# Performance work log

Hardware: AMD Instinct MI355X
Metric: run time of the kernel (lower is better)

The kernel has to match this reference:

```python
import jax, jax.numpy as jnp
import numpy as np

B, S, H, NH, DK, VOCAB, FF, L = 512, 64, 512, 8, 64, 2000, 2048, 6


def _pos_enc():
    pos = jnp.arange(S, dtype=jnp.float32)[:, None]           # [S,1]
    i = jnp.arange(H // 2, dtype=jnp.float32)                  # [H/2]
    ang = pos / (10000.0 ** (2.0 * i / H))                     # [S,H/2]
    pe = jnp.zeros((S, H), jnp.float32)
    pe = pe.at[:, 0::2].set(jnp.sin(ang)).at[:, 1::2].set(jnp.cos(ang))
    return pe


def _ln(x, g, b, eps=1e-5):
    m = x.mean(-1, keepdims=True)
    v = ((x - m) ** 2).mean(-1, keepdims=True)
    return (x - m) / jnp.sqrt(v + eps) * g + b


def _heads(x, w):  # x:[B,S,H] w:[H,H] -> [B,NH,S,DK]
    return (x @ w.T).reshape(B, S, NH, DK).transpose(0, 2, 1, 3)


def _sdpa(Q, K, V, keep):  # keep: bool mask broadcastable to [B,NH,S,S]
    scores = jnp.einsum('bhqd,bhkd->bhqk', Q, K) / np.sqrt(DK).astype(np.float32)
    scores = jnp.where(keep, scores, -1e9)
    return jnp.einsum('bhqk,bhkd->bhqd', jax.nn.softmax(scores, axis=-1), V)


def _merge(z, wo):  # [B,NH,S,DK] -> [B,S,H] -> out proj
    return z.transpose(0, 2, 1, 3).reshape(B, S, H) @ wo.T


def setup_inputs():
    key = jax.random.key(0)
    ks = jax.random.split(key, 30)
    n = lambda k, sh: jax.random.normal(k, sh, jnp.float32) * 0.02
    inp = {
        'source_ids': jax.random.randint(ks[0], (B, S), 0, VOCAB),
        'target_ids': jax.random.randint(ks[1], (B, S), 0, VOCAB),
        'source_mask': jnp.ones((B, S), jnp.int32),
        'target_mask': jnp.ones((B, S), jnp.int32),
        'src_emb': n(ks[2], (VOCAB, H)),
        'tgt_emb': n(ks[3], (VOCAB, H)),
        'enc_wq': n(ks[4], (L, H, H)), 'enc_wk': n(ks[5], (L, H, H)),
        'enc_wv': n(ks[6], (L, H, H)), 'enc_wo': n(ks[7], (L, H, H)),
        'enc_ln_g': jnp.ones((L, H), jnp.float32), 'enc_ln_b': jnp.zeros((L, H), jnp.float32),
        'enc_fc1_w': n(ks[8], (L, FF, H)), 'enc_fc1_b': jnp.zeros((L, FF), jnp.float32),
        'enc_fc2_w': n(ks[9], (L, H, FF)), 'enc_fc2_b': jnp.zeros((L, H), jnp.float32),
        'dec_mwq': n(ks[10], (L, H, H)), 'dec_mwk': n(ks[11], (L, H, H)),
        'dec_mwv': n(ks[12], (L, H, H)), 'dec_mwo': n(ks[13], (L, H, H)),
        'dec_cwq': n(ks[14], (L, H, H)), 'dec_cwo': n(ks[15], (L, H, H)),
        'dec_ln_g': jnp.ones((L, H), jnp.float32), 'dec_ln_b': jnp.zeros((L, H), jnp.float32),
        'dec_fc_w': n(ks[16], (L, H, H)), 'dec_fc_b': jnp.zeros((L, H), jnp.float32),
    }
    return inp


def reference(source_ids, target_ids, source_mask, target_mask, src_emb, tgt_emb,
              enc_wq, enc_wk, enc_wv, enc_wo, enc_ln_g, enc_ln_b,
              enc_fc1_w, enc_fc1_b, enc_fc2_w, enc_fc2_b,
              dec_mwq, dec_mwk, dec_mwv, dec_mwo, dec_cwq, dec_cwo,
              dec_ln_g, dec_ln_b, dec_fc_w, dec_fc_b):
    pe = _pos_enc()
    x = src_emb[source_ids] + pe              # [B,S,H]
    y = tgt_emb[target_ids] + pe
    src_keep = (source_mask != 0)[:, None, None, :]                 # [B,1,1,S]
    causal = jnp.tril(jnp.ones((S, S), bool))
    tgt_keep = (target_mask != 0)[:, None, None, :] & causal[None, None]  # [B,1,S,S]

    Kenc = Venc = None
    for l in range(L):
        Q, K, Vh = _heads(x, enc_wq[l]), _heads(x, enc_wk[l]), _heads(x, enc_wv[l])
        z = _merge(_sdpa(Q, K, Vh, src_keep), enc_wo[l])
        x = _ln(x + z, enc_ln_g[l], enc_ln_b[l])
        f = (x @ enc_fc1_w[l].T + enc_fc1_b[l]) @ enc_fc2_w[l].T + enc_fc2_b[l]
        x = _ln(x + f, enc_ln_g[l], enc_ln_b[l])
        Kenc, Venc = K, Vh  # last encoder block's K,V feed decoder cross-attn

    for l in range(L):
        Q, K, Vh = _heads(y, dec_mwq[l]), _heads(y, dec_mwk[l]), _heads(y, dec_mwv[l])
        z1 = _merge(_sdpa(Q, K, Vh, tgt_keep), dec_mwo[l])
        t1 = _ln(y + z1, dec_ln_g[l], dec_ln_b[l])
        Qc = _heads(t1, dec_cwq[l])
        # NOTE: original applies the TARGET mask to encoder keys (faithful)
        z2 = _merge(_sdpa(Qc, Kenc, Venc, tgt_keep), dec_cwo[l])
        t2 = _ln(t1 + z2, dec_ln_g[l], dec_ln_b[l])
        t3 = t2 @ dec_fc_w[l].T + dec_fc_b[l]
        y = _ln(t2 + t3, dec_ln_g[l], dec_ln_b[l])
    return y
```

## Files before the change

### kernel.cpp

```cpp
#include <hip/hip_runtime.h>

typedef unsigned short u16;
typedef u16 u16x8 __attribute__((ext_vector_type(8)));
typedef __bf16 bf16x8 __attribute__((ext_vector_type(8)));
typedef float f32x4 __attribute__((ext_vector_type(4)));

#define TTOK 32768
#define HD 512
#define FFD 2048
#define SLEN 64
#define EW 262144

__device__ __forceinline__ float b2f(u16 u) {
  union { float f; unsigned int i; } v; v.i = ((unsigned int)u) << 16; return v.f;
}
__device__ __forceinline__ u16 f2b(float f) {
  union { float f; unsigned int i; } v; v.f = f;
  unsigned int i = v.i;
  return (u16)((i + 0x7FFFu + ((i >> 16) & 1u)) >> 16);
}

__device__ __forceinline__ void gload16(const u16* g, u16* l) {
  __builtin_amdgcn_global_load_lds((const __attribute__((address_space(1))) void*)g,
                                   (__attribute__((address_space(3))) void*)l,
                                   16, 0, 0);
}

__device__ __forceinline__ f32x4 mfma16(bf16x8 a, bf16x8 b, f32x4 c) {
  return __builtin_amdgcn_mfma_f32_16x16x32_bf16(a, b, c, 0, 0, 0);
}

__global__ __launch_bounds__(256) void pe_kernel(float* __restrict__ pe) {
  int idx = blockIdx.x * 256 + threadIdx.x;
  int s = idx >> 9, h = idx & 511;
  float e2i = (float)(h & ~1);
  float ang = (float)s * powf(10000.0f, -e2i * (1.0f / 512.0f));
  pe[idx] = (h & 1) ? cosf(ang) : sinf(ang);
}

__global__ __launch_bounds__(256) void wconv_kernel(
    const float* __restrict__ src, u16* __restrict__ dst,
    unsigned int npl, unsigned int dstride) {
  size_t i = ((size_t)blockIdx.x * 256 + threadIdx.x) * 8;
  unsigned int l = (unsigned int)(i / npl);
  unsigned int r = (unsigned int)(i - (size_t)l * npl);
  f32x4 a = *(const f32x4*)(src + i), b = *(const f32x4*)(src + i + 4);
  u16x8 o;
  #pragma unroll
  for (int k = 0; k < 4; ++k) { o[k] = f2b(a[k]); o[4 + k] = f2b(b[k]); }
  *(u16x8*)(dst + (size_t)l * dstride + r) = o;
}

__global__ __launch_bounds__(256) void embed_kernel(
    const int* __restrict__ ids, const float* __restrict__ emb,
    const float* __restrict__ pe, u16* __restrict__ outB) {
  int chunk = blockIdx.x * 256 + threadIdx.x;
  int t = chunk >> 6;
  int c8 = (chunk & 63) * 8;
  int s = t & (SLEN - 1);
  int id = ids[t];
  const float* e = emb + (size_t)id * HD + c8;
  const float* p = pe + s * HD + c8;
  f32x4 e0 = *(const f32x4*)e, e1 = *(const f32x4*)(e + 4);
  f32x4 p0 = *(const f32x4*)p, p1 = *(const f32x4*)(p + 4);
  u16x8 ob;
  #pragma unroll
  for (int i = 0; i < 4; ++i) {
    ob[i]     = f2b(e0[i] + p0[i]);
    ob[4 + i] = f2b(e1[i] + p1[i]);
  }
  *(u16x8*)(outB + (size_t)t * HD + c8) = ob;
}

template<int F32OUT>
__global__ __launch_bounds__(256) void ln_kernel(
    const u16* A, const u16* __restrict__ Z, int ldz,
    const float* __restrict__ g, const float* __restrict__ b,
    u16* outB, float* outF) {
  int row = blockIdx.x * 4 + (threadIdx.x >> 6);
  int lane = threadIdx.x & 63;
  size_t base = (size_t)row * HD + lane * 8;
  size_t zbase = (size_t)row * ldz + lane * 8;
  u16x8 av = *(const u16x8*)(A + base);
  u16x8 zv = *(const u16x8*)(Z + zbase);
  float x[8];
  float s = 0.f;
  #pragma unroll
  for (int i = 0; i < 8; ++i) { x[i] = b2f(av[i]) + b2f(zv[i]); s += x[i]; }
  #pragma unroll
  for (int off = 32; off; off >>= 1) s += __shfl_xor(s, off);
  float m = s * (1.0f / HD);
  float vs = 0.f;
  #pragma unroll
  for (int i = 0; i < 8; ++i) { float d = x[i] - m; vs += d * d; }
  #pragma unroll
  for (int off = 32; off; off >>= 1) vs += __shfl_xor(vs, off);
  float rstd = rsqrtf(vs * (1.0f / HD) + 1e-5f);
  f32x4 g0 = *(const f32x4*)(g + lane * 8), g1 = *(const f32x4*)(g + lane * 8 + 4);
  f32x4 b0 = *(const f32x4*)(b + lane * 8), b1 = *(const f32x4*)(b + lane * 8 + 4);
  float o[8];
  #pragma unroll
  for (int i = 0; i < 4; ++i) {
    o[i]     = (x[i] - m) * rstd * g0[i] + b0[i];
    o[4 + i] = (x[4 + i] - m) * rstd * g1[i] + b1[i];
  }
  if (F32OUT) {
    f32x4 o0, o1;
    #pragma unroll
    for (int i = 0; i < 4; ++i) { o0[i] = o[i]; o1[i] = o[4 + i]; }
    *(f32x4*)(outF + base) = o0;
    *(f32x4*)(outF + base + 4) = o1;
  } else {
    u16x8 ob;
    #pragma unroll
    for (int i = 0; i < 8; ++i) ob[i] = f2b(o[i]);
    *(u16x8*)(outB + base) = ob;
  }
}

#define BAR() __builtin_amdgcn_s_barrier()
#define WAIT_LGKM0() asm volatile("s_waitcnt lgkmcnt(0)" ::: "memory")
#define WAIT_VM8()   asm volatile("s_waitcnt vmcnt(8)" ::: "memory")

template<int BIAS, int ACC>
__global__ __launch_bounds__(512, 2) void gemm256(
    const u16* __restrict__ A, const u16* __restrict__ Bw,
    const float* __restrict__ bias, u16* __restrict__ Cb,
    int nbn, int K, int lda, int ldb, int ldc) {
  __shared__ u16 lds[65536];
  const int tid = threadIdx.x;
  const int lane = tid & 63, w = tid >> 6;
  const int wr = w >> 2, wc = w & 3;
  const int l15 = lane & 15, lq = lane >> 4;

  const int cpx = gridDim.x >> 3;
  const int L = (blockIdx.x & 7) * cpx + (blockIdx.x >> 3);
  const int bm = (L / nbn) * 256, bn = (L % nbn) * 256;

  const u16 *pa0, *pa1, *pb0, *pb1;
  {
    int p0 = w * 1024 + lane * 16;
    int p1 = p0 + 8192;
    int lb0 = p0 ^ (((p0 >> 7) & 7) << 4);
    int lb1 = p1 ^ (((p1 >> 7) & 7) << 4);
    int r0 = (lb0 >> 7) + (((lb0 >> 6) & 1) << 7);
    int r1 = (lb1 >> 7) + (((lb1 >> 6) & 1) << 7);
    int c0 = (lb0 & 63) >> 1;
    int c1 = (lb1 & 63) >> 1;
    pa0 = A  + (size_t)(bm + r0) * lda + c0;
    pa1 = A  + (size_t)(bm + r1) * lda + c1;
    pb0 = Bw + (size_t)(bn + r0) * ldb + c0;
    pb1 = Bw + (size_t)(bn + r1) * ldb + c1;
  }
  const int dst = w * 512;

  int offA[8], offB[4];
  #pragma unroll
  for (int mf = 0; mf < 8; ++mf) {
    int rowp = mf * 16 + l15;
    offA[mf] = ((rowp * 128 + wr * 64 + lq * 16) ^ ((l15 & 7) << 4)) >> 1;
  }
  #pragma unroll
  for (int j = 0; j < 4; ++j) {
    int rB = wc * 64 + j * 16 + l15;
    int rowp = rB & 127, cg = rB >> 7;
    offB[j] = ((rowp * 128 + cg * 64 + lq * 16) ^ ((l15 & 7) << 4)) >> 1;
  }

  const int NK2 = K >> 5;
  const int NT  = K >> 6;

#define STAGEA(kh, slot) { \
    gload16(pa0 + (kh) * 32, &lds[(slot) * 8192 + dst]); \
    gload16(pa1 + (kh) * 32, &lds[(slot) * 8192 + dst + 4096]); }
#define STAGEB(kh, slot) { \
    gload16(pb0 + (kh) * 32, &lds[32768 + (slot) * 8192 + dst]); \
    gload16(pb1 + (kh) * 32, &lds[32768 + (slot) * 8192 + dst + 4096]); }
#define LDA4(slot, mh) { \
    _Pragma("unroll") for (int i = 0; i < 4; ++i) \
      af[i] = *(const bf16x8*)&lds[(slot) * 8192 + offA[(mh) * 4 + i]]; }
#define LDB4(slot) { \
    _Pragma("unroll") for (int j = 0; j < 4; ++j) \
      bf[j] = *(const bf16x8*)&lds[32768 + (slot) * 8192 + offB[j]]; }
#define MFMA16(mh) { \
    __builtin_amdgcn_s_setprio(1); \
    _Pragma("unroll") for (int i = 0; i < 4; ++i) \
      _Pragma("unroll") for (int j = 0; j < 4; ++j) \
        acc[(mh) * 4 + i][j] = mfma16(af[i], bf[j], acc[(mh) * 4 + i][j]); \
    __builtin_amdgcn_s_setprio(0); }

  f32x4 acc[8][4] = {};
  bf16x8 af[4], bf[4];

  STAGEA(0, 0); STAGEB(0, 0);
  STAGEA(1, 1); STAGEB(1, 1);
  STAGEA(2, 2); STAGEB(2, 2);
  WAIT_VM8();
  BAR();

  for (int t = 0; t < NT; ++t) {
    const int s0 = (2 * t) & 3, s1 = (2 * t + 1) & 3;
    int kh3 = 2 * t + 3; if (kh3 > NK2 - 1) kh3 = NK2 - 1;
    int kh4 = 2 * t + 4; if (kh4 > NK2 - 1) kh4 = NK2 - 1;
    const int w3 = (2 * t + 3) & 3, w4 = (2 * t + 4) & 3;

    LDB4(s0); LDA4(s0, 0);
    STAGEA(kh3, w3);
    BAR(); WAIT_LGKM0();
    MFMA16(0);
    BAR();

    LDA4(s0, 1);
    STAGEB(kh3, w3);
    BAR(); WAIT_LGKM0();
    MFMA16(1);
    WAIT_VM8();
    BAR();

    LDB4(s1); LDA4(s1, 0);
    STAGEA(kh4, w4);
    BAR(); WAIT_LGKM0();
    MFMA16(0);
    BAR();

    LDA4(s1, 1);
    STAGEB(kh4, w4);
    BAR(); WAIT_LGKM0();
    MFMA16(1);
    WAIT_VM8();
    BAR();
  }
  asm volatile("s_waitcnt vmcnt(0)" ::: "memory");

  #pragma unroll
  for (int h = 0; h < 2; ++h) {
    BAR();
    if (wr == h) {
      #pragma unroll
      for (int mf = 0; mf < 8; ++mf)
        #pragma unroll
        for (int j = 0; j < 4; ++j)
          #pragma unroll
          for (int r = 0; r < 4; ++r) {
            int row = mf * 16 + lq * 4 + r;
            int col = wc * 64 + j * 16 + l15;
            int byt = (row * 1024 + col * 4) ^ (((row >> 2) & 1) << 6);
            *(float*)((char*)lds + byt) = acc[mf][j][r];
          }
    }
    WAIT_LGKM0();
    BAR();
    #pragma unroll
    for (int k = 0; k < 8; ++k) {
      int c = tid + k * 512;
      int row = c >> 5, c32 = c & 31;
      int byt = (row * 1024 + c32 * 32) ^ (((row >> 2) & 1) << 6);
      f32x4 v0 = *(const f32x4*)((const char*)lds + byt);
      f32x4 v1 = *(const f32x4*)((const char*)lds + byt + 16);
      int gcol = bn + c32 * 8;
      size_t off = (size_t)(bm + h * 128 + row) * ldc + gcol;
      if (BIAS) {
        f32x4 bb0 = *(const f32x4*)(bias + gcol);
        f32x4 bb1 = *(const f32x4*)(bias + gcol + 4);
        #pragma unroll
        for (int i = 0; i < 4; ++i) { v0[i] += bb0[i]; v1[i] += bb1[i]; }
      }
      u16x8 ob;
      if (ACC) {
        u16x8 cr = *(const u16x8*)(Cb + off);
        #pragma unroll
        for (int i = 0; i < 4; ++i) {
          ob[i]     = f2b(v0[i] + b2f(cr[i]));
          ob[4 + i] = f2b(v1[i] + b2f(cr[4 + i]));
        }
      } else {
        #pragma unroll
        for (int i = 0; i < 4; ++i) { ob[i] = f2b(v0[i]); ob[4 + i] = f2b(v1[i]); }
      }
      *(u16x8*)(Cb + off) = ob;
    }
  }
#undef STAGEA
#undef STAGEB
#undef LDA4
#undef LDB4
#undef MFMA16
}

template<int CAUSAL, int SAVEKV>
__global__ __launch_bounds__(256) void attn_kernel(
    u16* Q, const u16* __restrict__ Kb, const u16* __restrict__ Vb,
    const int* __restrict__ mask, int qld, int kvld, u16* __restrict__ kvdst) {
  __shared__ u16 Ks[64 * 72];
  __shared__ u16 Vt[64 * 72];
  __shared__ u16 Ps[4][16 * 72];
  const int bh = blockIdx.x;
  const int b = bh >> 3, h = bh & 7;
  const int h0 = h * 64;
  const int tid = threadIdx.x, lane = tid & 63, w = tid >> 6;
  const size_t qbase = (size_t)b * 64 * qld + h0;
  const size_t kbase = (size_t)b * 64 * kvld + h0;
  const int l15 = lane & 15, l16 = (lane >> 4) * 8;

  {
    int r = tid >> 2;
    int c = (tid & 3) * 16;
    const u16* ksrc = Kb + kbase + (size_t)r * kvld + c;
    u16x8 k0 = *(const u16x8*)ksrc;
    u16x8 k1 = *(const u16x8*)(ksrc + 8);
    *(u16x8*)&Ks[r * 72 + c]     = k0;
    *(u16x8*)&Ks[r * 72 + c + 8] = k1;
    const u16* vsrc = Vb + kbase + (size_t)r * kvld + c;
    u16x8 t0 = *(const u16x8*)vsrc;
    u16x8 t1 = *(const u16x8*)(vsrc + 8);
    #pragma unroll
    for (int i = 0; i < 8; ++i) {
      Vt[(c + i) * 72 + r]     = t0[i];
      Vt[(c + 8 + i) * 72 + r] = t1[i];
    }
    if (SAVEKV) {
      size_t db = (size_t)(b * 64 + r) * 1024 + h0 + c;
      *(u16x8*)(kvdst + db)       = k0;
      *(u16x8*)(kvdst + db + 8)   = k1;
      *(u16x8*)(kvdst + db + 512) = t0;
      *(u16x8*)(kvdst + db + 520) = t1;
    }
  }
  const int qrow = w * 16 + l15;
  const u16* qp = Q + qbase + (size_t)qrow * qld;
  bf16x8 qf0 = *(const bf16x8*)&qp[l16];
  bf16x8 qf1 = *(const bf16x8*)&qp[32 + l16];
  __syncthreads();

  f32x4 sc[4] = {};
  #pragma unroll
  for (int nf = 0; nf < 4; ++nf) {
    bf16x8 k0 = *(const bf16x8*)&Ks[(nf * 16 + l15) * 72 + l16];
    bf16x8 k1 = *(const bf16x8*)&Ks[(nf * 16 + l15) * 72 + 32 + l16];
    sc[nf] = mfma16(qf0, k0, sc[nf]);
    sc[nf] = mfma16(qf1, k1, sc[nf]);
  }
  int mk[4];
  #pragma unroll
  for (int nf = 0; nf < 4; ++nf) mk[nf] = mask[b * 64 + nf * 16 + l15];
  float pv[4][4];
  #pragma unroll
  for (int r = 0; r < 4; ++r) {
    int q = w * 16 + (lane >> 4) * 4 + r;
    #pragma unroll
    for (int nf = 0; nf < 4; ++nf) {
      int k = nf * 16 + l15;
      bool kp = (mk[nf] != 0);
      if (CAUSAL) kp = kp && (k <= q);
      pv[r][nf] = kp ? sc[nf][r] * 0.125f : -1e9f;
    }
  }
  #pragma unroll
  for (int r = 0; r < 4; ++r) {
    float mx = fmaxf(fmaxf(pv[r][0], pv[r][1]), fmaxf(pv[r][2], pv[r][3]));
    #pragma unroll
    for (int off = 1; off < 16; off <<= 1) mx = fmaxf(mx, __shfl_xor(mx, off));
    float sum = 0.f;
    #pragma unroll
    for (int nf = 0; nf < 4; ++nf) { pv[r][nf] = __expf(pv[r][nf] - mx); sum += pv[r][nf]; }
    #pragma unroll
    for (int off = 1; off < 16; off <<= 1) sum += __shfl_xor(sum, off);
    float inv = 1.0f / sum;
    #pragma unroll
    for (int nf = 0; nf < 4; ++nf) pv[r][nf] *= inv;
  }
  #pragma unroll
  for (int r = 0; r < 4; ++r) {
    int q = (lane >> 4) * 4 + r;
    #pragma unroll
    for (int nf = 0; nf < 4; ++nf)
      Ps[w][q * 72 + nf * 16 + l15] = f2b(pv[r][nf]);
  }
  f32x4 oacc[4] = {};
  #pragma unroll
  for (int kk = 0; kk < 2; ++kk) {
    bf16x8 pa = *(const bf16x8*)&Ps[w][l15 * 72 + kk * 32 + l16];
    #pragma unroll
    for (int df = 0; df < 4; ++df) {
      bf16x8 vf = *(const bf16x8*)&Vt[(df * 16 + l15) * 72 + kk * 32 + l16];
      oacc[df] = mfma16(pa, vf, oacc[df]);
    }
  }
  #pragma unroll
  for (int df = 0; df < 4; ++df) {
    int col = df * 16 + l15;
    #pragma unroll
    for (int r = 0; r < 4; ++r) {
      int t = w * 16 + (lane >> 4) * 4 + r;
      Q[qbase + (size_t)t * qld + col] = f2b(oacc[df][r]);
    }
  }
}

extern "C" void kernel_launch(void* const* d_in, const int* in_sizes, int n_in,
                              void* d_out, int out_size, void* d_ws, size_t ws_size,
                              hipStream_t stream) {
  const int* src_ids    = (const int*)d_in[0];
  const int* tgt_ids    = (const int*)d_in[1];
  const int* src_mask   = (const int*)d_in[2];
  const int* tgt_mask   = (const int*)d_in[3];
  const float* src_emb  = (const float*)d_in[4];
  const float* tgt_emb  = (const float*)d_in[5];
  const float* enc_wq = (const float*)d_in[6];
  const float* enc_wk = (const float*)d_in[7];
  const float* enc_wv = (const float*)d_in[8];
  const float* enc_wo = (const float*)d_in[9];
  const float* enc_g  = (const float*)d_in[10];
  const float* enc_b  = (const float*)d_in[11];
  const float* fc1w = (const float*)d_in[12];
  const float* fc1b = (const float*)d_in[13];
  const float* fc2w = (const float*)d_in[14];
  const float* fc2b = (const float*)d_in[15];
  const float* mwq = (const float*)d_in[16];
  const float* mwk = (const float*)d_in[17];
  const float* mwv = (const float*)d_in[18];
  const float* mwo = (const float*)d_in[19];
  const float* cwq = (const float*)d_in[20];
  const float* cwo = (const float*)d_in[21];
  const float* dec_g = (const float*)d_in[22];
  const float* dec_b = (const float*)d_in[23];
  const float* dfw = (const float*)d_in[24];
  const float* dfb = (const float*)d_in[25];
  float* outF = (float*)d_out;
  u16* kvenc = (u16*)d_out;

  constexpr size_t SZ_PE  = (size_t)SLEN * HD * 4;
  constexpr size_t SZ_W   = (size_t)114 * EW * 2;
  constexpr size_t SZ_CUR = (size_t)TTOK * HD * 2;
  constexpr size_t SZ_QKV = (size_t)TTOK * 1536 * 2;
  constexpr size_t SZ_R   = (size_t)TTOK * FFD * 2;
  constexpr size_t SZ_Z2  = (size_t)TTOK * HD * 2;
  constexpr size_t NEED_SMALL = SZ_PE + SZ_W + SZ_CUR + SZ_QKV;
  constexpr size_t NEED_BIG   = SZ_PE + SZ_W + SZ_CUR + SZ_R + SZ_Z2;
  if (ws_size < NEED_SMALL) return;
  const bool big = (ws_size >= NEED_BIG);

  char* ws = (char*)d_ws;
  float* pe = (float*)ws;
  u16* W    = (u16*)(ws + SZ_PE);
  u16* cur  = (u16*)(ws + SZ_PE + SZ_W);
  u16* qkv  = (u16*)(ws + SZ_PE + SZ_W + SZ_CUR);
  u16* z2   = big ? (u16*)(ws + SZ_PE + SZ_W + SZ_CUR + SZ_R)
                  : qkv + (size_t)TTOK * 1024;

  dim3 blk(256), blk5(512);
  const unsigned int E = EW, S_E = 12 * EW, S_D = 7 * EW;
  u16* WD = W + (size_t)72 * EW;

  pe_kernel<<<128, blk, 0, stream>>>(pe);

  wconv_kernel<<<768,  blk, 0, stream>>>(enc_wq, W,          E,     S_E);
  wconv_kernel<<<768,  blk, 0, stream>>>(enc_wk, W + E,      E,     S_E);
  wconv_kernel<<<768,  blk, 0, stream>>>(enc_wv, W + 2 * E,  E,     S_E);
  wconv_kernel<<<768,  blk, 0, stream>>>(enc_wo, W + 3 * E,  E,     S_E);
  wconv_kernel<<<3072, blk, 0, stream>>>(fc1w,   W + 4 * E,  4 * E, S_E);
  wconv_kernel<<<3072, blk, 0, stream>>>(fc2w,   W + 8 * E,  4 * E, S_E);
  wconv_kernel<<<768,  blk, 0, stream>>>(mwq,    WD,         E,     S_D);
  wconv_kernel<<<768,  blk, 0, stream>>>(mwk,    WD + E,     E,     S_D);
  wconv_kernel<<<768,  blk, 0, stream>>>(mwv,    WD + 2 * E, E,     S_D);
  wconv_kernel<<<768,  blk, 0, stream>>>(mwo,    WD + 3 * E, E,     S_D);
  wconv_kernel<<<768,  blk, 0, stream>>>(cwq,    WD + 4 * E, E,     S_D);
  wconv_kernel<<<768,  blk, 0, stream>>>(cwo,    WD + 5 * E, E,     S_D);
  wconv_kernel<<<768,  blk, 0, stream>>>(dfw,    WD + 6 * E, E,     S_D);

  embed_kernel<<<8192, blk, 0, stream>>>(src_ids, src_emb, pe, cur);
  for (int l = 0; l < 6; ++l) {
    const u16* Wl = W + (size_t)l * S_E;
    const float* g  = enc_g + (size_t)l * HD;
    const float* bb = enc_b + (size_t)l * HD;
    const float* b1 = fc1b + (size_t)l * FFD;
    const float* b2 = fc2b + (size_t)l * HD;

    gemm256<0,0><<<768, blk5, 0, stream>>>(cur, Wl, nullptr, qkv, 6, 512, 512, 512, 1536);
    if (l == 5)
      attn_kernel<0,1><<<4096, blk, 0, stream>>>(qkv, qkv + 512, qkv + 1024, src_mask, 1536, 1536, kvenc);
    else
      attn_kernel<0,0><<<4096, blk, 0, stream>>>(qkv, qkv + 512, qkv + 1024, src_mask, 1536, 1536, nullptr);
    gemm256<0,0><<<256, blk5, 0, stream>>>(qkv, Wl + 3 * E, nullptr, qkv + 1024, 2, 512, 1536, 512, 1536);
    ln_kernel<0><<<8192, blk, 0, stream>>>(cur, qkv + 1024, 1536, g, bb, cur, nullptr);
    if (big) {
      gemm256<1,0><<<1024, blk5, 0, stream>>>(cur, Wl + 4 * E, b1, qkv, 8, 512, 512, 512, 2048);
      gemm256<1,0><<<256,  blk5, 0, stream>>>(qkv, Wl + 8 * E, b2, z2, 2, 2048, 2048, 2048, 512);
    } else {
      gemm256<1,0><<<512, blk5, 0, stream>>>(cur, Wl + 4 * E, b1,        qkv, 4, 512, 512, 512, 1024);
      gemm256<1,0><<<256, blk5, 0, stream>>>(qkv, Wl + 8 * E, b2,        z2,  2, 1024, 1024, 2048, 512);
      gemm256<1,0><<<512, blk5, 0, stream>>>(cur, Wl + 6 * E, b1 + 1024, qkv, 4, 512, 512, 512, 1024);
      gemm256<0,1><<<256, blk5, 0, stream>>>(qkv, Wl + 8 * E + 1024, nullptr, z2, 2, 1024, 1024, 2048, 512);
    }
    ln_kernel<0><<<8192, blk, 0, stream>>>(cur, z2, 512, g, bb, cur, nullptr);
  }

  embed_kernel<<<8192, blk, 0, stream>>>(tgt_ids, tgt_emb, pe, cur);
  for (int l = 0; l < 6; ++l) {
    const u16* Wl = WD + (size_t)l * S_D;
    const float* g  = dec_g + (size_t)l * HD;
    const float* bb = dec_b + (size_t)l * HD;
    const float* fb = dfb + (size_t)l * HD;

    gemm256<0,0><<<768, blk5, 0, stream>>>(cur, Wl, nullptr, qkv, 6, 512, 512, 512, 1536);
    attn_kernel<1,0><<<4096, blk, 0, stream>>>(qkv, qkv + 512, qkv + 1024, tgt_mask, 1536, 1536, nullptr);
    gemm256<0,0><<<256, blk5, 0, stream>>>(qkv, Wl + 3 * E, nullptr, qkv + 1024, 2, 512, 1536, 512, 1536);
    ln_kernel<0><<<8192, blk, 0, stream>>>(cur, qkv + 1024, 1536, g, bb, cur, nullptr);

    gemm256<0,0><<<256, blk5, 0, stream>>>(cur, Wl + 4 * E, nullptr, qkv, 2, 512, 512, 512, 1536);
    attn_kernel<1,0><<<4096, blk, 0, stream>>>(qkv, kvenc, kvenc + 512, tgt_mask, 1536, 1024, nullptr);
    gemm256<0,0><<<256, blk5, 0, stream>>>(qkv, Wl + 5 * E, nullptr, qkv + 1024, 2, 512, 1536, 512, 1536);
    ln_kernel<0><<<8192, blk, 0, stream>>>(cur, qkv + 1024, 1536, g, bb, cur, nullptr);

    gemm256<1,0><<<256, blk5, 0, stream>>>(cur, Wl + 6 * E, fb, qkv, 2, 512, 512, 512, 512);
    if (l == 5)
      ln_kernel<1><<<8192, blk, 0, stream>>>(cur, qkv, 512, g, bb, nullptr, outF);
    else
      ln_kernel<0><<<8192, blk, 0, stream>>>(cur, qkv, 512, g, bb, cur, nullptr);
  }
  (void)in_sizes; (void)n_in; (void)out_size;
}
```

Before: 3.528 ms.

## Fuse N=512 projection GEMMs with residual-add LayerNorm epilogue

Adds a gemm_ln kernel that computes a full 128x512 row tile per block, so each block holds complete rows and can apply bias, residual add and LayerNorm in the epilogue. It replaces the gemm256 plus ln_kernel pairs for the attention output projections, FFN second layer and decoder FC when the 'big' path is taken. This removes a round trip of the intermediate through global memory and one launch per fused pair. In exchange the new kernel uses a simpler double-buffered pipeline with 128-row tiles, which may give lower MFMA efficiency than the 256x256 kernel, and it writes its output in place over the residual buffer.

```diff
diff --git a/kernel.cpp b/kernel.cpp
--- a/kernel.cpp
+++ b/kernel.cpp
@@ -121,6 +121,8 @@
 #define BAR() __builtin_amdgcn_s_barrier()
 #define WAIT_LGKM0() asm volatile("s_waitcnt lgkmcnt(0)" ::: "memory")
 #define WAIT_VM8()   asm volatile("s_waitcnt vmcnt(8)" ::: "memory")
+#define WAIT_VM5()   asm volatile("s_waitcnt vmcnt(5)" ::: "memory")
+#define WAIT_VM0()   asm volatile("s_waitcnt vmcnt(0)" ::: "memory")
 
 template<int BIAS, int ACC>
 __global__ __launch_bounds__(512, 2) void gemm256(
@@ -230,7 +232,7 @@
     WAIT_VM8();
     BAR();
   }
-  asm volatile("s_waitcnt vmcnt(0)" ::: "memory");
+  WAIT_VM0();
 
   #pragma unroll
   for (int h = 0; h < 2; ++h) {
@@ -285,6 +287,160 @@
 #undef LDA4
 #undef LDB4
 #undef MFMA16
+}
+
+template<int BIAS, int F32OUT>
+__global__ __launch_bounds__(512, 2) void gemm_ln(
+    const u16* __restrict__ A, const u16* __restrict__ Bw,
+    const float* __restrict__ bias,
+    const u16* __restrict__ resid, const float* __restrict__ g,
+    const float* __restrict__ bv,
+    u16* outB, float* outF, int K, int lda, int ldb) {
+  __shared__ u16 lds[40960];
+  const int tid = threadIdx.x;
+  const int lane = tid & 63, w = tid >> 6;
+  const int l15 = lane & 15, lq = lane >> 4;
+
+  const int cpx = gridDim.x >> 3;
+  const int L = (blockIdx.x & 7) * cpx + (blockIdx.x >> 3);
+  const int bm = L * 128;
+
+  const u16* pa;
+  const u16* pb[4];
+  {
+    int p = tid * 16;
+    int row = p >> 6;
+    int lb = ((((p >> 4) & 3) ^ ((row >> 2) & 3)) << 4) | (p & 15);
+    pa = A + (size_t)(bm + row) * lda + (lb >> 1);
+    #pragma unroll
+    for (int c = 0; c < 4; ++c) {
+      int q = c * 8192 + tid * 16;
+      int rowb = q >> 6;
+      int lbb = ((((q >> 4) & 3) ^ ((rowb >> 2) & 3)) << 4) | (q & 15);
+      pb[c] = Bw + (size_t)rowb * ldb + (lbb >> 1);
+    }
+  }
+
+  int offA[8], offB[4];
+  #pragma unroll
+  for (int mf = 0; mf < 8; ++mf) {
+    int row = mf * 16 + l15;
+    offA[mf] = row * 32 + ((lq ^ ((row >> 2) & 3)) << 3);
+  }
+  #pragma unroll
+  for (int j = 0; j < 4; ++j) {
+    int row = w * 64 + j * 16 + l15;
+    offB[j] = row * 32 + ((lq ^ ((row >> 2) & 3)) << 3);
+  }
+
+  const int NS = K >> 5;
+
+#define STAGE(s, sl) { \
+    gload16(pa + (s) * 32, &lds[(sl) * 4096 + w * 512]); \
+    _Pragma("unroll") for (int c = 0; c < 4; ++c) \
+      gload16(pb[c] + (s) * 32, &lds[8192 + (sl) * 16384 + c * 4096 + w * 512]); }
+
+  f32x4 acc[8][4] = {};
+
+  STAGE(0, 0);
+  for (int h = 0; h < NS; ++h) {
+    int nh = h + 1; if (nh > NS - 1) nh = NS - 1;
+    STAGE(nh, (h + 1) & 1);
+    WAIT_VM5();
+    BAR();
+    const int sa = (h & 1) * 4096, sb = 8192 + (h & 1) * 16384;
+    bf16x8 af[8], bf4[4];
+    #pragma unroll
+    for (int i = 0; i < 8; ++i) af[i] = *(const bf16x8*)&lds[sa + offA[i]];
+    #pragma unroll
+    for (int j = 0; j < 4; ++j) bf4[j] = *(const bf16x8*)&lds[sb + offB[j]];
+    WAIT_LGKM0();
+    __builtin_amdgcn_s_setprio(1);
+    #pragma unroll
+    for (int mf = 0; mf < 8; ++mf)
+      #pragma unroll
+      for (int j = 0; j < 4; ++j)
+        acc[mf][j] = mfma16(af[mf], bf4[j], acc[mf][j]);
+    __builtin_amdgcn_s_setprio(0);
+    BAR();
+  }
+  WAIT_VM0();
+
+  float bias4[4] = {0.f, 0.f, 0.f, 0.f};
+  if (BIAS) {
+    #pragma unroll
+    for (int j = 0; j < 4; ++j) bias4[j] = bias[w * 64 + j * 16 + l15];
+  }
+  const f32x4 gv0 = *(const f32x4*)(g + lane * 8);
+  const f32x4 gv1 = *(const f32x4*)(g + lane * 8 + 4);
+  const f32x4 bv0 = *(const f32x4*)(bv + lane * 8);
+  const f32x4 bv1 = *(const f32x4*)(bv + lane * 8 + 4);
+
+  #pragma unroll
+  for (int q = 0; q < 4; ++q) {
+    BAR();
+    #pragma unroll
+    for (int mi = 0; mi < 2; ++mi) {
+      int mf = 2 * q + mi;
+      #pragma unroll
+      for (int j = 0; j < 4; ++j)
+        #pragma unroll
+        for (int r = 0; r < 4; ++r) {
+          int lrow = mi * 16 + lq * 4 + r;
+          int col = w * 64 + j * 16 + l15;
+          int byt = (lrow * 2048 + col * 4) ^ (((lrow >> 2) & 3) << 6);
+          *(float*)((char*)lds + byt) = acc[mf][j][r] + bias4[j];
+        }
+    }
+    WAIT_LGKM0();
+    BAR();
+    #pragma unroll
+    for (int rr = 0; rr < 4; ++rr) {
+      int lrow = w * 4 + rr;
+      int grow = bm + q * 32 + lrow;
+      int byt = (lrow * 2048 + lane * 32) ^ (((lrow >> 2) & 3) << 6);
+      f32x4 z0 = *(const f32x4*)((const char*)lds + byt);
+      f32x4 z1 = *(const f32x4*)((const char*)lds + byt + 16);
+      u16x8 av = *(const u16x8*)(resid + (size_t)grow * HD + lane * 8);
+      float x[8];
+      float s = 0.f;
+      #pragma unroll
+      for (int i = 0; i < 4; ++i) {
+        x[i] = b2f(av[i]) + z0[i];
+        x[4 + i] = b2f(av[4 + i]) + z1[i];
+      }
+      #pragma unroll
+      for (int i = 0; i < 8; ++i) s += x[i];
+      #pragma unroll
+      for (int off = 32; off; off >>= 1) s += __shfl_xor(s, off);
+      float m = s * (1.0f / HD);
+      float vs = 0.f;
+      #pragma unroll
+      for (int i = 0; i < 8; ++i) { float d = x[i] - m; vs += d * d; }
+      #pragma unroll
+      for (int off = 32; off; off >>= 1) vs += __shfl_xor(vs, off);
+      float rstd = rsqrtf(vs * (1.0f / HD) + 1e-5f);
+      float o[8];
+      #pragma unroll
+      for (int i = 0; i < 4; ++i) {
+        o[i]     = (x[i] - m) * rstd * gv0[i] + bv0[i];
+        o[4 + i] = (x[4 + i] - m) * rstd * gv1[i] + bv1[i];
+      }
+      if (F32OUT) {
+        f32x4 o0, o1;
+        #pragma unroll
+        for (int i = 0; i < 4; ++i) { o0[i] = o[i]; o1[i] = o[4 + i]; }
+        *(f32x4*)(outF + (size_t)grow * HD + lane * 8) = o0;
+        *(f32x4*)(outF + (size_t)grow * HD + lane * 8 + 4) = o1;
+      } else {
+        u16x8 ob;
+        #pragma unroll
+        for (int i = 0; i < 8; ++i) ob[i] = f2b(o[i]);
+        *(u16x8*)(outB + (size_t)grow * HD + lane * 8) = ob;
+      }
+    }
+  }
+#undef STAGE
 }
 
 template<int CAUSAL, int SAVEKV>
@@ -481,18 +637,19 @@
       attn_kernel<0,1><<<4096, blk, 0, stream>>>(qkv, qkv + 512, qkv + 1024, src_mask, 1536, 1536, kvenc);
     else
       attn_kernel<0,0><<<4096, blk, 0, stream>>>(qkv, qkv + 512, qkv + 1024, src_mask, 1536, 1536, nullptr);
-    gemm256<0,0><<<256, blk5, 0, stream>>>(qkv, Wl + 3 * E, nullptr, qkv + 1024, 2, 512, 1536, 512, 1536);
-    ln_kernel<0><<<8192, blk, 0, stream>>>(cur, qkv + 1024, 1536, g, bb, cur, nullptr);
     if (big) {
+      gemm_ln<0,0><<<256, blk5, 0, stream>>>(qkv, Wl + 3 * E, nullptr, cur, g, bb, cur, nullptr, 512, 1536, 512);
       gemm256<1,0><<<1024, blk5, 0, stream>>>(cur, Wl + 4 * E, b1, qkv, 8, 512, 512, 512, 2048);
-      gemm256<1,0><<<256,  blk5, 0, stream>>>(qkv, Wl + 8 * E, b2, z2, 2, 2048, 2048, 2048, 512);
+      gemm_ln<1,0><<<256, blk5, 0, stream>>>(qkv, Wl + 8 * E, b2, cur, g, bb, cur, nullptr, 2048, 2048, 2048);
     } else {
+      gemm256<0,0><<<256, blk5, 0, stream>>>(qkv, Wl + 3 * E, nullptr, qkv + 1024, 2, 512, 1536, 512, 1536);
+      ln_kernel<0><<<8192, blk, 0, stream>>>(cur, qkv + 1024, 1536, g, bb, cur, nullptr);
       gemm256<1,0><<<512, blk5, 0, stream>>>(cur, Wl + 4 * E, b1,        qkv, 4, 512, 512, 512, 1024);
       gemm256<1,0><<<256, blk5, 0, stream>>>(qkv, Wl + 8 * E, b2,        z2,  2, 1024, 1024, 2048, 512);
       gemm256<1,0><<<512, blk5, 0, stream>>>(cur, Wl + 6 * E, b1 + 1024, qkv, 4, 512, 512, 512, 1024);
       gemm256<0,1><<<256, blk5, 0, stream>>>(qkv, Wl + 8 * E + 1024, nullptr, z2, 2, 1024, 1024, 2048, 512);
-    }
-    ln_kernel<0><<<8192, blk, 0, stream>>>(cur, z2, 512, g, bb, cur, nullptr);
+      ln_kernel<0><<<8192, blk, 0, stream>>>(cur, z2, 512, g, bb, cur, nullptr);
+    }
   }
 
   embed_kernel<<<8192, blk, 0, stream>>>(tgt_ids, tgt_emb, pe, cur);
@@ -504,19 +661,28 @@
 
     gemm256<0,0><<<768, blk5, 0, stream>>>(cur, Wl, nullptr, qkv, 6, 512, 512, 512, 1536);
     attn_kernel<1,0><<<4096, blk, 0, stream>>>(qkv, qkv + 512, qkv + 1024, tgt_mask, 1536, 1536, nullptr);
-    gemm256<0,0><<<256, blk5, 0, stream>>>(qkv, Wl + 3 * E, nullptr, qkv + 1024, 2, 512, 1536, 512, 1536);
-    ln_kernel<0><<<8192, blk, 0, stream>>>(cur, qkv + 1024, 1536, g, bb, cur, nullptr);
-
-    gemm256<0,0><<<256, blk5, 0, stream>>>(cur, Wl + 4 * E, nullptr, qkv, 2, 512, 512, 512, 1536);
-    attn_kernel<1,0><<<4096, blk, 0, stream>>>(qkv, kvenc, kvenc + 512, tgt_mask, 1536, 1024, nullptr);
-    gemm256<0,0><<<256, blk5, 0, stream>>>(qkv, Wl + 5 * E, nullptr, qkv + 1024, 2, 512, 1536, 512, 1536);
-    ln_kernel<0><<<8192, blk, 0, stream>>>(cur, qkv + 1024, 1536, g, bb, cur, nullptr);
-
-    gemm256<1,0><<<256, blk5, 0, stream>>>(cur, Wl + 6 * E, fb, qkv, 2, 512, 512, 512, 512);
-    if (l == 5)
-      ln_kernel<1><<<8192, blk, 0, stream>>>(cur, qkv, 512, g, bb, nullptr, outF);
-    else
-      ln_kernel<0><<<8192, blk, 0, stream>>>(cur, qkv, 512, g, bb, cur, nullptr);
+    if (big) {
+      gemm_ln<0,0><<<256, blk5, 0, stream>>>(qkv, Wl + 3 * E, nullptr, cur, g, bb, cur, nullptr, 512, 1536, 512);
+      gemm256<0,0><<<256, blk5, 0, stream>>>(cur, Wl + 4 * E, nullptr, qkv, 2, 512, 512, 512, 1536);
+      attn_kernel<1,0><<<4096, blk, 0, stream>>>(qkv, kvenc, kvenc + 512, tgt_mask, 1536, 1024, nullptr);
+      gemm_ln<0,0><<<256, blk5, 0, stream>>>(qkv, Wl + 5 * E, nullptr, cur, g, bb, cur, nullptr, 512, 1536, 512);
+      if (l == 5)
+        gemm_ln<1,1><<<256, blk5, 0, stream>>>(cur, Wl + 6 * E, fb, cur, g, bb, nullptr, outF, 512, 512, 512);
+      else
+        gemm_ln<1,0><<<256, blk5, 0, stream>>>(cur, Wl + 6 * E, fb, cur, g, bb, cur, nullptr, 512, 512, 512);
+    } else {
+      gemm256<0,0><<<256, blk5, 0, stream>>>(qkv, Wl + 3 * E, nullptr, qkv + 1024, 2, 512, 1536, 512, 1536);
+      ln_kernel<0><<<8192, blk, 0, stream>>>(cur, qkv + 1024, 1536, g, bb, cur, nullptr);
+      gemm256<0,0><<<256, blk5, 0, stream>>>(cur, Wl + 4 * E, nullptr, qkv, 2, 512, 512, 512, 1536);
+      attn_kernel<1,0><<<4096, blk, 0, stream>>>(qkv, kvenc, kvenc + 512, tgt_mask, 1536, 1024, nullptr);
+      gemm256<0,0><<<256, blk5, 0, stream>>>(qkv, Wl + 5 * E, nullptr, qkv + 1024, 2, 512, 1536, 512, 1536);
+      ln_kernel<0><<<8192, blk, 0, stream>>>(cur, qkv + 1024, 1536, g, bb, cur, nullptr);
+      gemm256<1,0><<<256, blk5, 0, stream>>>(cur, Wl + 6 * E, fb, qkv, 2, 512, 512, 512, 512);
+      if (l == 5)
+        ln_kernel<1><<<8192, blk, 0, stream>>>(cur, qkv, 512, g, bb, nullptr, outF);
+      else
+        ln_kernel<0><<<8192, blk, 0, stream>>>(cur, qkv, 512, g, bb, cur, nullptr);
+    }
   }
   (void)in_sizes; (void)n_in; (void)out_size;
 }
```

Result: no change. 3.473 ms (-1.6%).
